# Kernel tuning notes

Hardware: AMD Instinct MI355X
Metric: run time of the kernel (lower is better)

Reference implementation:

```python
import jax, jax.numpy as jnp
import numpy as np
import math

V, D, H, L, MLP = 32000, 1024, 16, 4, 4
B, T = 2, 1024
HD = D // H
ALIBI_BIAS_MAX = 8.0
EPS = 1e-5


def _ln(x, g, b):
    m = jnp.mean(x, -1, keepdims=True)
    v = jnp.mean((x - m) ** 2, -1, keepdims=True)
    return (x - m) * jax.lax.rsqrt(v + EPS) * g + b


def setup_inputs() -> dict:
    key = jax.random.key(0)
    ks = jax.random.split(key, 12)
    s = 0.02
    inp = {
        "input_ids": jax.random.randint(ks[0], (B, T), 0, V),
        "wte": jax.random.normal(ks[1], (V, D), jnp.float32) * s,
        "ln1_g": jnp.ones((L, D), jnp.float32),
        "ln1_b": jnp.zeros((L, D), jnp.float32),
        "attn_w": jax.random.normal(ks[2], (L, 3 * D, D), jnp.float32) * s,
        "attn_b": jnp.zeros((L, 3 * D), jnp.float32),
        "proj_w": jax.random.normal(ks[3], (L, D, D), jnp.float32) * s,
        "proj_b": jnp.zeros((L, D), jnp.float32),
        "ln2_g": jnp.ones((L, D), jnp.float32),
        "ln2_b": jnp.zeros((L, D), jnp.float32),
        "fc_w": jax.random.normal(ks[4], (L, MLP * D, D), jnp.float32) * s,
        "fc_b": jnp.zeros((L, MLP * D), jnp.float32),
        "fc2_w": jax.random.normal(ks[5], (L, D, MLP * D), jnp.float32) * s,
        "fc2_b": jnp.zeros((L, D), jnp.float32),
        "lnf_g": jnp.ones((D,), jnp.float32),
        "lnf_b": jnp.zeros((D,), jnp.float32),
        "lm_head_w": jax.random.normal(ks[6], (V, D), jnp.float32) * s,
    }
    return inp


def reference(input_ids, wte, ln1_g, ln1_b, attn_w, attn_b, proj_w, proj_b,
              ln2_g, ln2_b, fc_w, fc_b, fc2_w, fc2_b, lnf_g, lnf_b, lm_head_w):
    b, t = input_ids.shape
    x = wte[input_ids]  # [B,T,D]

    # causal + ALiBi bias, [H,T,T]
    pos = jnp.arange(t)
    rel = -jnp.abs(pos[None, :] - pos[:, None]).astype(jnp.float32)  # -|i-j|
    m = jnp.arange(1, H + 1, dtype=jnp.float32) * (ALIBI_BIAS_MAX / H)
    alibi = rel[None, :, :] * (2.0 ** (-m))[:, None, None]
    causal = jnp.where(pos[None, :] > pos[:, None], -jnp.inf, 0.0)
    bias = alibi + causal[None]
    scale = 1.0 / math.sqrt(HD)

    def block(x, p):
        l1g, l1b, aw, ab, pw, pb, l2g, l2b, fw, fb, f2w, f2b = p
        h = _ln(x, l1g, l1b)
        qkv = h @ aw.T + ab  # [B,T,3D]
        q, k, v = jnp.split(qkv, 3, axis=-1)
        q = q.reshape(b, t, H, HD).transpose(0, 2, 1, 3)
        k = k.reshape(b, t, H, HD).transpose(0, 2, 1, 3)
        v = v.reshape(b, t, H, HD).transpose(0, 2, 1, 3)
        att = jnp.einsum('bhid,bhjd->bhij', q, k) * scale + bias[None]
        att = jax.nn.softmax(att, axis=-1)
        y = jnp.einsum('bhij,bhjd->bhid', att, v)
        y = y.transpose(0, 2, 1, 3).reshape(b, t, D)
        x = x + (y @ pw.T + pb)
        h2 = _ln(x, l2g, l2b)
        x = x + (jax.nn.gelu(h2 @ fw.T + fb, approximate=False) @ f2w.T + f2b)
        return x, None

    x, _ = jax.lax.scan(
        block, x,
        (ln1_g, ln1_b, attn_w, attn_b, proj_w, proj_b,
         ln2_g, ln2_b, fc_w, fc_b, fc2_w, fc2_b))
    x = _ln(x, lnf_g, lnf_b)
    logits = x @ lm_head_w.T  # [B,T,V]
    return logits
```

## Files before the change

### kernel.cpp

```cpp
#include <hip/hip_runtime.h>
#include <hip/hip_bf16.h>
#include <math.h>

typedef __hip_bfloat16 bf16;
typedef __attribute__((ext_vector_type(4))) float f32x4;
typedef __attribute__((ext_vector_type(8))) short short8;

constexpr int Bc = 2, Tc = 1024, Dc = 1024, Hc = 16, Lc = 4, MLPc = 4096, Vc = 32000, HDc = 64;

__device__ __forceinline__ unsigned short f2bu(float f) {
    __hip_bfloat16 h = __float2bfloat16(f);
    unsigned short u;
    __builtin_memcpy(&u, &h, 2);
    return u;
}

__device__ __forceinline__ void gl2lds16(const bf16* g, bf16* l) {
    __builtin_amdgcn_global_load_lds(
        (const __attribute__((address_space(1))) void*)g,
        (__attribute__((address_space(3))) void*)l, 16, 0, 0);
}

enum { EPI_BIAS_BF16 = 0, EPI_GELU = 1, EPI_RESADD = 2, EPI_F32 = 3, EPI_QKV = 4 };

template <int EPI>
__device__ __forceinline__ void epi_store(float v, int row, int col, void* Cv,
                                          int ldc, const float* bias) {
    if constexpr (EPI == EPI_BIAS_BF16) {
        v += bias[col];
        ((bf16*)Cv)[(size_t)row * ldc + col] = __float2bfloat16(v);
    } else if constexpr (EPI == EPI_GELU) {
        v += bias[col];
        v = 0.5f * v * (1.0f + erff(v * 0.70710678118f));
        ((bf16*)Cv)[(size_t)row * ldc + col] = __float2bfloat16(v);
    } else if constexpr (EPI == EPI_RESADD) {
        float* C = (float*)Cv;
        size_t idx = (size_t)row * ldc + col;
        C[idx] += v + bias[col];
    } else if constexpr (EPI == EPI_F32) {
        ((float*)Cv)[(size_t)row * ldc + col] = v;
    } else if constexpr (EPI == EPI_QKV) {
        v += bias[col];
        bf16 bv = __float2bfloat16(v);
        int b = row >> 10, t = row & 1023;
        int seg = col >> 10;
        int cc = col & 1023;
        int h = cc >> 6, hd = cc & 63;
        bf16* base = (bf16*)Cv;
        if (seg == 0)
            base[((size_t)(b * Hc + h) * Tc + t) * HDc + hd] = bv;
        else if (seg == 1)
            base[2097152 + ((size_t)(b * Hc + h) * Tc + t) * HDc + hd] = bv;
        else
            base[4194304 + ((size_t)(b * Hc + h) * HDc + hd) * Tc + t] = bv;
    }
}

template <int MH>
__device__ __forceinline__ void load_af8(short8 (&af)[4][2], const char* Abase,
                                         int wm, int lr, int lq) {
#pragma unroll
    for (int fi = 0; fi < 4; fi++) {
        int r = MH * 128 + wm * 64 + fi * 16 + lr;
#pragma unroll
        for (int kk = 0; kk < 2; kk++) {
            int cb = (kk * 64 + lq * 16) ^ ((r & 7) << 4);
            af[fi][kk] = *reinterpret_cast<const short8*>(Abase + (size_t)r * 128 + cb);
        }
    }
}
template <int NH>
__device__ __forceinline__ void load_bf4(short8 (&bfv)[2][2], const char* Bbase,
                                         int wn, int lr, int lq) {
#pragma unroll
    for (int fj = 0; fj < 2; fj++) {
        int r = NH * 128 + wn * 32 + fj * 16 + lr;
#pragma unroll
        for (int kk = 0; kk < 2; kk++) {
            int cb = (kk * 64 + lq * 16) ^ ((r & 7) << 4);
            bfv[fj][kk] = *reinterpret_cast<const short8*>(Bbase + (size_t)r * 128 + cb);
        }
    }
}
template <int MH, int NH>
__device__ __forceinline__ void mma16(f32x4 (&acc)[2][2][4][2],
                                      const short8 (&af)[4][2], const short8 (&bfv)[2][2]) {
#pragma unroll
    for (int kk = 0; kk < 2; kk++)
#pragma unroll
        for (int fi = 0; fi < 4; fi++)
#pragma unroll
            for (int fj = 0; fj < 2; fj++)
                acc[MH][NH][fi][fj] = __builtin_amdgcn_mfma_f32_16x16x32_bf16(
                    af[fi][kk], bfv[fj][kk], acc[MH][NH][fi][fj], 0, 0, 0);
}

template <int EPI>
__global__ __launch_bounds__(512) void gemm_8p(
    const bf16* __restrict__ A, int lda,
    const bf16* __restrict__ Bm, int ldb,
    void* __restrict__ Cv, int ldc,
    const float* __restrict__ bias, int K)
{
    constexpr int BM = 256, BN = 256, BK = 64;
    __shared__ alignas(16) bf16 As[2][BM][BK];
    __shared__ alignas(16) bf16 Bs[2][BN][BK];

    const int tid = threadIdx.x;
    const int lane = tid & 63;
    const int w = tid >> 6;
    const int wm = w >> 2;
    const int wn = w & 3;

    int nwg = gridDim.x * gridDim.y;
    int orig = blockIdx.y * gridDim.x + blockIdx.x;
    int q = nwg >> 3, rr = nwg & 7, xcd = orig & 7, lid = orig >> 3;
    int wg = (xcd < rr ? xcd * (q + 1) : rr * (q + 1) + (xcd - rr) * q) + lid;
    int im = wg % gridDim.x;
    int in = wg / gridDim.x;

    const bf16* Ab = A + (size_t)im * BM * lda;
    const bf16* Bb = Bm + (size_t)in * BN * ldb;

    const int sr = lane >> 3;
    const int scs = ((lane & 7) ^ sr) * 8;
    const int lr = lane & 15, lq = lane >> 4;

    f32x4 acc[2][2][4][2];
#pragma unroll
    for (int a = 0; a < 2; a++)
#pragma unroll
        for (int b = 0; b < 2; b++)
#pragma unroll
            for (int c = 0; c < 4; c++)
#pragma unroll
                for (int d = 0; d < 2; d++) acc[a][b][c][d] = (f32x4){0.f, 0.f, 0.f, 0.f};

    const int NT = K / BK;

    auto stage_half = [&](int buf, int sg, int k0) {
        const bool isB = (sg == 1 || sg == 2);
        const bf16* gp = isB ? Bb : Ab;
        const int ld = isB ? ldb : lda;
        bf16* ls = isB ? &Bs[buf][0][0] : &As[buf][0][0];
        const int half = (sg == 2 || sg == 3) ? 1 : 0;
#pragma unroll
        for (int i = 0; i < 2; i++) {
            int r0 = half * 128 + i * 64 + w * 8;
            gl2lds16(gp + (size_t)(r0 + sr) * ld + k0 + scs, ls + r0 * BK);
        }
    };

#pragma unroll
    for (int sg = 0; sg < 4; sg++) stage_half(0, sg, 0);
    asm volatile("s_waitcnt vmcnt(0)" ::: "memory");
    __builtin_amdgcn_s_barrier();
    asm volatile("" ::: "memory");

    short8 af[4][2], bfv[2][2];

    for (int t = 0; t < NT; t++) {
        const int cur = t & 1;
        const char* Abase = (const char*)&As[cur][0][0];
        const char* Bbase = (const char*)&Bs[cur][0][0];
        const bool pf = (t + 1 < NT);
        const int kn = (t + 1) * BK;

        load_af8<0>(af, Abase, wm, lr, lq);
        load_bf4<0>(bfv, Bbase, wn, lr, lq);
        if (pf) stage_half(cur ^ 1, 0, kn);
        __builtin_amdgcn_s_barrier();
        __builtin_amdgcn_s_setprio(1);
        mma16<0, 0>(acc, af, bfv);
        __builtin_amdgcn_s_setprio(0);
        asm volatile("s_waitcnt vmcnt(4)" ::: "memory");
        __builtin_amdgcn_s_barrier();

        load_bf4<1>(bfv, Bbase, wn, lr, lq);
        if (pf) stage_half(cur ^ 1, 1, kn);
        __builtin_amdgcn_s_barrier();
        __builtin_amdgcn_s_setprio(1);
        mma16<0, 1>(acc, af, bfv);
        __builtin_amdgcn_s_setprio(0);
        asm volatile("s_waitcnt vmcnt(4)" ::: "memory");
        __builtin_amdgcn_s_barrier();

        load_af8<1>(af, Abase, wm, lr, lq);
        if (pf) stage_half(cur ^ 1, 2, kn);
        __builtin_amdgcn_s_barrier();
        __builtin_amdgcn_s_setprio(1);
        mma16<1, 1>(acc, af, bfv);
        __builtin_amdgcn_s_setprio(0);
        asm volatile("" ::: "memory");
        __builtin_amdgcn_s_barrier();

        load_bf4<0>(bfv, Bbase, wn, lr, lq);
        if (pf) stage_half(cur ^ 1, 3, kn);
        __builtin_amdgcn_s_barrier();
        __builtin_amdgcn_s_setprio(1);
        mma16<1, 0>(acc, af, bfv);
        __builtin_amdgcn_s_setprio(0);
        asm volatile("s_waitcnt vmcnt(4)" ::: "memory");
        __builtin_amdgcn_s_barrier();
    }

#pragma unroll
    for (int mh = 0; mh < 2; mh++)
#pragma unroll
        for (int nh = 0; nh < 2; nh++)
#pragma unroll
            for (int fi = 0; fi < 4; fi++)
#pragma unroll
                for (int fj = 0; fj < 2; fj++)
#pragma unroll
                    for (int r = 0; r < 4; r++) {
                        int row = im * 256 + mh * 128 + wm * 64 + fi * 16 + lq * 4 + r;
                        int col = in * 256 + nh * 128 + wn * 32 + fj * 16 + lr;
                        epi_store<EPI>(acc[mh][nh][fi][fj][r], row, col, Cv, ldc, bias);
                    }
}

template <int BM, int BN, int BK, int EPI, bool SWZG>
__global__ __launch_bounds__(256) void gemm_fast(
    const bf16* __restrict__ A, int lda,
    const bf16* __restrict__ Bm, int ldb,
    void* __restrict__ Cv, int ldc,
    const float* __restrict__ bias, int K)
{
    static_assert(BK == 64, "staging geometry assumes BK=64");
    __shared__ alignas(16) bf16 As[2][BM][BK];
    __shared__ alignas(16) bf16 Bs[2][BN][BK];

    const int tid = threadIdx.x;
    const int lane = tid & 63;
    const int w = tid >> 6;
    const int wm = w >> 1, wn = w & 1;
    constexpr int WM = BM / 2, WN = BN / 2;
    constexpr int FM = WM / 16, FN = WN / 16;
    constexpr int RPI = 512 / BK;
    constexpr int AI = BM / (4 * RPI);
    constexpr int BI = BN / (4 * RPI);

    int im, in;
    if constexpr (SWZG) {
        int nwg = gridDim.x * gridDim.y;
        int orig = blockIdx.y * gridDim.x + blockIdx.x;
        int q = nwg >> 3, rr = nwg & 7, xcd = orig & 7, lid = orig >> 3;
        int wg = (xcd < rr ? xcd * (q + 1) : rr * (q + 1) + (xcd - rr) * q) + lid;
        im = wg % gridDim.x;
        in = wg / gridDim.x;
    } else {
        im = blockIdx.y;
        in = blockIdx.x;
    }

    const bf16* Ab = A + (size_t)im * BM * lda;
    const bf16* Bb = Bm + (size_t)in * BN * ldb;

    const int sr = lane >> 3;
    const int scs = (((lane & 7) ^ sr) * 8);
    const int lr = lane & 15, lq = lane >> 4;

    f32x4 acc[FM][FN];
#pragma unroll
    for (int i = 0; i < FM; i++)
#pragma unroll
        for (int j = 0; j < FN; j++) acc[i][j] = (f32x4){0.f, 0.f, 0.f, 0.f};

    auto stage = [&](int buf, int k0) {
#pragma unroll
        for (int i = 0; i < AI; i++) {
            int row = (w * AI + i) * RPI;
            gl2lds16(Ab + (size_t)(row + sr) * lda + k0 + scs, &As[buf][row][0]);
        }
#pragma unroll
        for (int i = 0; i < BI; i++) {
            int row = (w * BI + i) * RPI;
            gl2lds16(Bb + (size_t)(row + sr) * ldb + k0 + scs, &Bs[buf][row][0]);
        }
    };

    const int NT = K / BK;
    stage(0, 0);
    __syncthreads();

    for (int t = 0; t < NT; t++) {
        const int cur = t & 1;
        if (t + 1 < NT) stage(cur ^ 1, (t + 1) * BK);

        const char* Abase = (const char*)&As[cur][0][0];
        const char* Bbase = (const char*)&Bs[cur][0][0];
#pragma unroll
        for (int kk = 0; kk < BK / 32; kk++) {
            short8 af[FM], bfr[FN];
#pragma unroll
            for (int i = 0; i < FM; i++) {
                int r = wm * WM + i * 16 + lr;
                int cb = (kk * 64 + lq * 16) ^ ((r & 7) << 4);
                af[i] = *reinterpret_cast<const short8*>(Abase + (size_t)r * (BK * 2) + cb);
            }
#pragma unroll
            for (int j = 0; j < FN; j++) {
                int r = wn * WN + j * 16 + lr;
                int cb = (kk * 64 + lq * 16) ^ ((r & 7) << 4);
                bfr[j] = *reinterpret_cast<const short8*>(Bbase + (size_t)r * (BK * 2) + cb);
            }
#pragma unroll
            for (int i = 0; i < FM; i++)
#pragma unroll
                for (int j = 0; j < FN; j++)
                    acc[i][j] = __builtin_amdgcn_mfma_f32_16x16x32_bf16(af[i], bfr[j], acc[i][j], 0, 0, 0);
        }
        __syncthreads();
    }

#pragma unroll
    for (int i = 0; i < FM; i++)
#pragma unroll
        for (int j = 0; j < FN; j++)
#pragma unroll
            for (int r = 0; r < 4; r++) {
                int row = im * BM + wm * WM + i * 16 + lq * 4 + r;
                int col = in * BN + wn * WN + j * 16 + lr;
                epi_store<EPI>(acc[i][j][r], row, col, Cv, ldc, bias);
            }
}

template <int BM, int BN, int BK, int EPI>
__global__ __launch_bounds__(256) void gemm_bt_f32(
    const bf16* __restrict__ A, int lda,
    const float* __restrict__ Bm, int ldb,
    void* __restrict__ Cv, int ldc,
    const float* __restrict__ bias, int K)
{
    constexpr int BKP = BK + 8;
    __shared__ bf16 As[BM][BKP];
    __shared__ bf16 Bs[BN][BKP];
    const int tid = threadIdx.x;
    const int lane = tid & 63;
    const int w = tid >> 6;
    const int wm = w >> 1, wn = w & 1;
    constexpr int WM = BM / 2, WN = BN / 2;
    constexpr int FM = WM / 16, FN = WN / 16;
    const int bx = blockIdx.x, by = blockIdx.y;
    const bf16* Ab = A + (size_t)by * BM * lda;
    const float* Bb = Bm + (size_t)bx * BN * ldb;
    f32x4 acc[FM][FN];
#pragma unroll
    for (int i = 0; i < FM; i++)
#pragma unroll
        for (int j = 0; j < FN; j++) acc[i][j] = (f32x4){0.f, 0.f, 0.f, 0.f};
    const int lr = lane & 15, lq = lane >> 4;
    for (int k0 = 0; k0 < K; k0 += BK) {
        constexpr int AC = (BM * BK) / (256 * 8);
#pragma unroll
        for (int i = 0; i < AC; i++) {
            int c = tid + i * 256;
            int row = c / (BK / 8);
            int kc = (c % (BK / 8)) * 8;
            *reinterpret_cast<int4*>(&As[row][kc]) =
                *reinterpret_cast<const int4*>(Ab + (size_t)row * lda + k0 + kc);
        }
        constexpr int BC = (BN * BK) / (256 * 4);
#pragma unroll
        for (int i = 0; i < BC; i++) {
            int c = tid + i * 256;
            int row = c / (BK / 4);
            int kc = (c % (BK / 4)) * 4;
            float4 v = *reinterpret_cast<const float4*>(Bb + (size_t)row * ldb + k0 + kc);
            unsigned long long p = (unsigned long long)f2bu(v.x) |
                                   ((unsigned long long)f2bu(v.y) << 16) |
                                   ((unsigned long long)f2bu(v.z) << 32) |
                                   ((unsigned long long)f2bu(v.w) << 48);
            *reinterpret_cast<unsigned long long*>(&Bs[row][kc]) = p;
        }
        __syncthreads();
#pragma unroll
        for (int kk = 0; kk < BK / 32; kk++) {
            short8 af[FM], bfr[FN];
#pragma unroll
            for (int i = 0; i < FM; i++)
                af[i] = *reinterpret_cast<const short8*>(&As[wm * WM + i * 16 + lr][kk * 32 + lq * 8]);
#pragma unroll
            for (int j = 0; j < FN; j++)
                bfr[j] = *reinterpret_cast<const short8*>(&Bs[wn * WN + j * 16 + lr][kk * 32 + lq * 8]);
#pragma unroll
            for (int i = 0; i < FM; i++)
#pragma unroll
                for (int j = 0; j < FN; j++)
                    acc[i][j] = __builtin_amdgcn_mfma_f32_16x16x32_bf16(af[i], bfr[j], acc[i][j], 0, 0, 0);
        }
        __syncthreads();
    }
#pragma unroll
    for (int i = 0; i < FM; i++)
#pragma unroll
        for (int j = 0; j < FN; j++)
#pragma unroll
            for (int r = 0; r < 4; r++) {
                int row = by * BM + wm * WM + i * 16 + lq * 4 + r;
                int col = bx * BN + wn * WN + j * 16 + lr;
                epi_store<EPI>(acc[i][j][r], row, col, Cv, ldc, bias);
            }
}

__global__ __launch_bounds__(256) void flash_attn(
    const bf16* __restrict__ q, const bf16* __restrict__ kbuf,
    const bf16* __restrict__ vt, bf16* __restrict__ y)
{
    __shared__ alignas(16) bf16 Ks[128 * 64];
    __shared__ alignas(16) bf16 Vs[64 * 128];
    __shared__ alignas(16) bf16 Ps[4 * 16 * 136];

    const int tid = threadIdx.x;
    const int lane = tid & 63;
    const int w = tid >> 6;
    const int lr = lane & 15, lq = lane >> 4;
    const int qi = (int)gridDim.x - 1 - (int)blockIdx.x;
    const int z = blockIdx.y;
    const int b = z >> 4, h = z & 15;
    const float slope = exp2f(-0.5f * (float)(h + 1));

    const bf16* qz = q + (size_t)z * (Tc * HDc);
    const bf16* kz = kbuf + (size_t)z * (Tc * HDc);
    const bf16* vz = vt + (size_t)z * (HDc * Tc);

    const int rowbase = qi * 64 + w * 16;

    short8 qf[2];
#pragma unroll
    for (int kk = 0; kk < 2; kk++)
        qf[kk] = *reinterpret_cast<const short8*>(
            qz + (size_t)(rowbase + lr) * HDc + kk * 32 + lq * 8);

    float m_old[4], l_sum[4];
#pragma unroll
    for (int r = 0; r < 4; r++) { m_old[r] = -3.0e38f; l_sum[r] = 0.f; }
    f32x4 o[4];
#pragma unroll
    for (int dj = 0; dj < 4; dj++) o[dj] = (f32x4){0.f, 0.f, 0.f, 0.f};

    bf16* Pw = Ps + w * 16 * 136;

    const int nkv = (qi * 64 + 63) / 128 + 1;
    for (int kv = 0; kv < nkv; kv++) {
#pragma unroll
        for (int i = 0; i < 4; i++) {
            int rbase = w * 32 + i * 8;
            int row = rbase + (lane >> 3);
            int slot = lane & 7;
            gl2lds16(kz + (size_t)(kv * 128 + row) * HDc + ((slot ^ (row & 7)) * 8),
                     &Ks[rbase * 64]);
        }
#pragma unroll
        for (int i = 0; i < 4; i++) {
            int rbase = w * 16 + i * 4;
            int row = rbase + lq;
            gl2lds16(vz + (size_t)row * Tc + kv * 128 + ((lr ^ (row & 7)) * 8),
                     &Vs[rbase * 128]);
        }
        __syncthreads();

        f32x4 s[8];
#pragma unroll
        for (int j = 0; j < 8; j++) s[j] = (f32x4){0.f, 0.f, 0.f, 0.f};
#pragma unroll
        for (int kk = 0; kk < 2; kk++) {
#pragma unroll
            for (int j = 0; j < 8; j++) {
                int row = j * 16 + lr;
                int cb = ((kk * 4 + lq) ^ (row & 7)) << 4;
                short8 bfr = *reinterpret_cast<const short8*>(
                    (const char*)Ks + row * 128 + cb);
                s[j] = __builtin_amdgcn_mfma_f32_16x16x32_bf16(qf[kk], bfr, s[j], 0, 0, 0);
            }
        }

        float mt[4];
#pragma unroll
        for (int r = 0; r < 4; r++) mt[r] = -3.0e38f;
#pragma unroll
        for (int j = 0; j < 8; j++) {
            int col = kv * 128 + j * 16 + lr;
#pragma unroll
            for (int r = 0; r < 4; r++) {
                int rowg = rowbase + lq * 4 + r;
                float v = s[j][r] * 0.125f - (float)(rowg - col) * slope;
                v = (col > rowg) ? -3.0e38f : v;
                s[j][r] = v;
                mt[r] = fmaxf(mt[r], v);
            }
        }
#pragma unroll
        for (int r = 0; r < 4; r++)
#pragma unroll
            for (int off = 1; off < 16; off <<= 1)
                mt[r] = fmaxf(mt[r], __shfl_xor(mt[r], off));

        float f[4], rs[4];
#pragma unroll
        for (int r = 0; r < 4; r++) {
            float mn = fmaxf(m_old[r], mt[r]);
            f[r] = __expf(m_old[r] - mn);
            m_old[r] = mn;
            rs[r] = 0.f;
        }
#pragma unroll
        for (int j = 0; j < 8; j++)
#pragma unroll
            for (int r = 0; r < 4; r++) {
                float p = __expf(s[j][r] - m_old[r]);
                s[j][r] = p;
                rs[r] += p;
            }
#pragma unroll
        for (int r = 0; r < 4; r++) {
#pragma unroll
            for (int off = 1; off < 16; off <<= 1)
                rs[r] += __shfl_xor(rs[r], off);
            l_sum[r] = l_sum[r] * f[r] + rs[r];
        }

#pragma unroll
        for (int j = 0; j < 8; j++)
#pragma unroll
            for (int r = 0; r < 4; r++)
                Pw[(lq * 4 + r) * 136 + j * 16 + lr] = __float2bfloat16(s[j][r]);

#pragma unroll
        for (int dj = 0; dj < 4; dj++)
#pragma unroll
            for (int r = 0; r < 4; r++) o[dj][r] *= f[r];

        __syncthreads();

#pragma unroll
        for (int kk = 0; kk < 4; kk++) {
            short8 pa = *reinterpret_cast<const short8*>(
                (const char*)Pw + lr * 272 + kk * 64 + lq * 16);
#pragma unroll
            for (int dj = 0; dj < 4; dj++) {
                int row = dj * 16 + lr;
                int cb = ((kk * 4 + lq) ^ (row & 7)) << 4;
                short8 vb = *reinterpret_cast<const short8*>(
                    (const char*)Vs + row * 256 + cb);
                o[dj] = __builtin_amdgcn_mfma_f32_16x16x32_bf16(pa, vb, o[dj], 0, 0, 0);
            }
        }
        __syncthreads();
    }

#pragma unroll
    for (int dj = 0; dj < 4; dj++)
#pragma unroll
        for (int r = 0; r < 4; r++) {
            int rowg = rowbase + lq * 4 + r;
            float outv = o[dj][r] / l_sum[r];
            y[((size_t)b * Tc + rowg) * Dc + h * HDc + dj * 16 + lr] =
                __float2bfloat16(outv);
        }
}

__global__ __launch_bounds__(256) void f2b8(const float* __restrict__ in,
                                            bf16* __restrict__ out, long n) {
    long i = ((long)blockIdx.x * 256 + threadIdx.x) * 8;
    if (i >= n) return;
    float4 a = *reinterpret_cast<const float4*>(in + i);
    float4 b = *reinterpret_cast<const float4*>(in + i + 4);
    unsigned long long p0 = (unsigned long long)f2bu(a.x) |
                            ((unsigned long long)f2bu(a.y) << 16) |
                            ((unsigned long long)f2bu(a.z) << 32) |
                            ((unsigned long long)f2bu(a.w) << 48);
    unsigned long long p1 = (unsigned long long)f2bu(b.x) |
                            ((unsigned long long)f2bu(b.y) << 16) |
                            ((unsigned long long)f2bu(b.z) << 32) |
                            ((unsigned long long)f2bu(b.w) << 48);
    *reinterpret_cast<unsigned long long*>(out + i) = p0;
    *reinterpret_cast<unsigned long long*>(out + i + 4) = p1;
}

__global__ __launch_bounds__(256) void embed_kernel(const int* __restrict__ ids,
                                                    const float* __restrict__ wte,
                                                    float* __restrict__ x) {
    int row = blockIdx.x;
    int t = threadIdx.x;
    int id = ids[row];
    reinterpret_cast<float4*>(x + (size_t)row * Dc)[t] =
        reinterpret_cast<const float4*>(wte + (size_t)id * Dc)[t];
}

__global__ __launch_bounds__(256) void ln_kernel(const float* __restrict__ x,
                                                 const float* __restrict__ g,
                                                 const float* __restrict__ b,
                                                 bf16* __restrict__ out) {
    int row = blockIdx.x;
    int t = threadIdx.x;
    const float4 v = reinterpret_cast<const float4*>(x + (size_t)row * Dc)[t];
    float s = v.x + v.y + v.z + v.w;
    float s2 = v.x * v.x + v.y * v.y + v.z * v.z + v.w * v.w;
#pragma unroll
    for (int o = 32; o > 0; o >>= 1) {
        s += __shfl_down(s, o);
        s2 += __shfl_down(s2, o);
    }
    __shared__ float sm[8];
    int wid = t >> 6, ln = t & 63;
    if (ln == 0) { sm[wid] = s; sm[4 + wid] = s2; }
    __syncthreads();
    if (t == 0) {
        float ts = sm[0] + sm[1] + sm[2] + sm[3];
        float ts2 = sm[4] + sm[5] + sm[6] + sm[7];
        sm[0] = ts; sm[4] = ts2;
    }
    __syncthreads();
    float mean = sm[0] * (1.0f / Dc);
    float var = sm[4] * (1.0f / Dc) - mean * mean;
    float rstd = rsqrtf(var + 1e-5f);
    int c0 = t * 4;
    float vv[4] = {v.x, v.y, v.z, v.w};
    unsigned long long p = 0;
#pragma unroll
    for (int j = 0; j < 4; j++) {
        float val = (vv[j] - mean) * rstd * g[c0 + j] + b[c0 + j];
        p |= (unsigned long long)f2bu(val) << (16 * j);
    }
    *reinterpret_cast<unsigned long long*>(out + (size_t)row * Dc + c0) = p;
}

extern "C" void kernel_launch(void* const* d_in, const int* in_sizes, int n_in,
                              void* d_out, int out_size, void* d_ws, size_t ws_size,
                              hipStream_t stream) {
    const int* ids = (const int*)d_in[0];
    const float* wte = (const float*)d_in[1];
    const float* ln1g = (const float*)d_in[2];
    const float* ln1b = (const float*)d_in[3];
    const float* attw = (const float*)d_in[4];
    const float* attb = (const float*)d_in[5];
    const float* projw = (const float*)d_in[6];
    const float* projb = (const float*)d_in[7];
    const float* ln2g = (const float*)d_in[8];
    const float* ln2b = (const float*)d_in[9];
    const float* fcw = (const float*)d_in[10];
    const float* fcb = (const float*)d_in[11];
    const float* fc2w = (const float*)d_in[12];
    const float* fc2b = (const float*)d_in[13];
    const float* lnfg = (const float*)d_in[14];
    const float* lnfb = (const float*)d_in[15];
    const float* lmw = (const float*)d_in[16];

    const int M = Bc * Tc;
    char* ws = (char*)d_ws;
    size_t off = 0;
    auto carve = [&](size_t bytes) { char* p = ws + off; off += (bytes + 255) & ~(size_t)255; return p; };

    float* x = (float*)carve((size_t)M * Dc * 4);
    bf16* h = (bf16*)carve((size_t)M * Dc * 2);
    bf16* q = (bf16*)carve((size_t)Bc * Hc * Tc * HDc * 2);
    bf16* kb = (bf16*)carve((size_t)Bc * Hc * Tc * HDc * 2);
    bf16* vt = (bf16*)carve((size_t)Bc * Hc * Tc * HDc * 2);
    bf16* y = (bf16*)carve((size_t)M * Dc * 2);
    bf16* mlp = (bf16*)carve((size_t)M * MLPc * 2);
    (void)kb; (void)vt;

    const long nLM = (long)Vc * Dc;
    bool has_wlm = ws_size >= off + (size_t)nLM * 2;
    bf16* wlm = nullptr;
    if (has_wlm) wlm = (bf16*)carve((size_t)nLM * 2);

    const long nAW = (long)Lc * 3 * Dc * Dc;
    const long nPW = (long)Lc * Dc * Dc;
    const long nFW = (long)Lc * MLPc * Dc;
    const long nF2W = (long)Lc * Dc * MLPc;
    bf16* awAll = (bf16*)d_out;
    bf16* pwAll = awAll + nAW;
    bf16* fwAll = pwAll + nPW;
    bf16* f2wAll = fwAll + nFW;

    embed_kernel<<<M, 256, 0, stream>>>(ids, wte, x);

    f2b8<<<(int)(nAW / 8 / 256), 256, 0, stream>>>(attw, awAll, nAW);
    f2b8<<<(int)(nPW / 8 / 256), 256, 0, stream>>>(projw, pwAll, nPW);
    f2b8<<<(int)(nFW / 8 / 256), 256, 0, stream>>>(fcw, fwAll, nFW);
    f2b8<<<(int)(nF2W / 8 / 256), 256, 0, stream>>>(fc2w, f2wAll, nF2W);
    if (has_wlm)
        f2b8<<<(int)(nLM / 8 / 256), 256, 0, stream>>>(lmw, wlm, nLM);

    for (int l = 0; l < Lc; l++) {
        bf16* aw_b = awAll + (size_t)l * 3 * Dc * Dc;
        bf16* pw_b = pwAll + (size_t)l * Dc * Dc;
        bf16* fw_b = fwAll + (size_t)l * MLPc * Dc;
        bf16* f2w_b = f2wAll + (size_t)l * Dc * MLPc;

        ln_kernel<<<M, 256, 0, stream>>>(x, ln1g + l * Dc, ln1b + l * Dc, h);

        gemm_fast<128, 128, 64, EPI_QKV, true>
            <<<dim3(M / 128, 3 * Dc / 128, 1), 256, 0, stream>>>(
                h, Dc, aw_b, Dc, q, 0, attb + l * 3 * Dc, Dc);

        flash_attn<<<dim3(Tc / 64, Bc * Hc), 256, 0, stream>>>(q, kb, vt, y);

        gemm_fast<128, 128, 64, EPI_RESADD, true>
            <<<dim3(M / 128, Dc / 128, 1), 256, 0, stream>>>(
                y, Dc, pw_b, Dc, x, Dc, projb + l * Dc, Dc);

        ln_kernel<<<M, 256, 0, stream>>>(x, ln2g + l * Dc, ln2b + l * Dc, h);

        gemm_fast<128, 128, 64, EPI_GELU, true>
            <<<dim3(M / 128, MLPc / 128, 1), 256, 0, stream>>>(
                h, Dc, fw_b, Dc, mlp, MLPc, fcb + l * MLPc, Dc);

        gemm_fast<128, 128, 64, EPI_RESADD, true>
            <<<dim3(M / 128, Dc / 128, 1), 256, 0, stream>>>(
                mlp, MLPc, f2w_b, MLPc, x, Dc, fc2b + l * Dc, MLPc);
    }

    ln_kernel<<<M, 256, 0, stream>>>(x, lnfg, lnfb, h);

    if (has_wlm)
        gemm_8p<EPI_F32>
            <<<dim3(M / 256, Vc / 256, 1), 512, 0, stream>>>(
                h, Dc, wlm, Dc, (float*)d_out, Vc, nullptr, Dc);
    else
        gemm_bt_f32<128, 128, 64, EPI_F32>
            <<<dim3(Vc / 128, M / 128, 1), 256, 0, stream>>>(
                h, Dc, lmw, Dc, (float*)d_out, Vc, nullptr, Dc);
}
```

Measured before the change: 1.282 ms.

## Store residual stream in bf16, add V transpose kernel, reuse B fragments

The residual stream x moves from fp32 to bf16 storage, so embed, layernorm and the residual-add epilogues read and write half the bytes. The QKV epilogue now writes V in the same row-major layout as Q and K, and a separate v2vt kernel transposes it for flash attention instead of doing strided scattered stores. The GEMM main loop keeps two B fragment register sets, which removes one LDS reload per k-step at the cost of more registers. Rounding the residual to bf16 after every layer adds accumulated precision error against the fp32 reference.

```diff
diff --git a/kernel.cpp b/kernel.cpp
--- a/kernel.cpp
+++ b/kernel.cpp
@@ -13,6 +13,11 @@
     unsigned short u;
     __builtin_memcpy(&u, &h, 2);
     return u;
+}
+__device__ __forceinline__ float bu2f(unsigned short u) {
+    __hip_bfloat16 h;
+    __builtin_memcpy(&h, &u, 2);
+    return __bfloat162float(h);
 }
 
 __device__ __forceinline__ void gl2lds16(const bf16* g, bf16* l) {
@@ -34,9 +39,10 @@
         v = 0.5f * v * (1.0f + erff(v * 0.70710678118f));
         ((bf16*)Cv)[(size_t)row * ldc + col] = __float2bfloat16(v);
     } else if constexpr (EPI == EPI_RESADD) {
-        float* C = (float*)Cv;
+        bf16* C = (bf16*)Cv;
         size_t idx = (size_t)row * ldc + col;
-        C[idx] += v + bias[col];
+        float xo = __bfloat162float(C[idx]);
+        C[idx] = __float2bfloat16(xo + v + bias[col]);
     } else if constexpr (EPI == EPI_F32) {
         ((float*)Cv)[(size_t)row * ldc + col] = v;
     } else if constexpr (EPI == EPI_QKV) {
@@ -47,12 +53,7 @@
         int cc = col & 1023;
         int h = cc >> 6, hd = cc & 63;
         bf16* base = (bf16*)Cv;
-        if (seg == 0)
-            base[((size_t)(b * Hc + h) * Tc + t) * HDc + hd] = bv;
-        else if (seg == 1)
-            base[2097152 + ((size_t)(b * Hc + h) * Tc + t) * HDc + hd] = bv;
-        else
-            base[4194304 + ((size_t)(b * Hc + h) * HDc + hd) * Tc + t] = bv;
+        base[(size_t)seg * 2097152 + ((size_t)(b * Hc + h) * Tc + t) * HDc + hd] = bv;
     }
 }
 
@@ -157,7 +158,7 @@
     __builtin_amdgcn_s_barrier();
     asm volatile("" ::: "memory");
 
-    short8 af[4][2], bfv[2][2];
+    short8 af[4][2], bfv0[2][2], bfv1[2][2];
 
     for (int t = 0; t < NT; t++) {
         const int cur = t & 1;
@@ -167,20 +168,20 @@
         const int kn = (t + 1) * BK;
 
         load_af8<0>(af, Abase, wm, lr, lq);
-        load_bf4<0>(bfv, Bbase, wn, lr, lq);
+        load_bf4<0>(bfv0, Bbase, wn, lr, lq);
         if (pf) stage_half(cur ^ 1, 0, kn);
         __builtin_amdgcn_s_barrier();
         __builtin_amdgcn_s_setprio(1);
-        mma16<0, 0>(acc, af, bfv);
+        mma16<0, 0>(acc, af, bfv0);
         __builtin_amdgcn_s_setprio(0);
         asm volatile("s_waitcnt vmcnt(4)" ::: "memory");
         __builtin_amdgcn_s_barrier();
 
-        load_bf4<1>(bfv, Bbase, wn, lr, lq);
+        load_bf4<1>(bfv1, Bbase, wn, lr, lq);
         if (pf) stage_half(cur ^ 1, 1, kn);
         __builtin_amdgcn_s_barrier();
         __builtin_amdgcn_s_setprio(1);
-        mma16<0, 1>(acc, af, bfv);
+        mma16<0, 1>(acc, af, bfv1);
         __builtin_amdgcn_s_setprio(0);
         asm volatile("s_waitcnt vmcnt(4)" ::: "memory");
         __builtin_amdgcn_s_barrier();
@@ -189,16 +190,15 @@
         if (pf) stage_half(cur ^ 1, 2, kn);
         __builtin_amdgcn_s_barrier();
         __builtin_amdgcn_s_setprio(1);
-        mma16<1, 1>(acc, af, bfv);
+        mma16<1, 1>(acc, af, bfv1);
         __builtin_amdgcn_s_setprio(0);
         asm volatile("" ::: "memory");
         __builtin_amdgcn_s_barrier();
 
-        load_bf4<0>(bfv, Bbase, wn, lr, lq);
         if (pf) stage_half(cur ^ 1, 3, kn);
         __builtin_amdgcn_s_barrier();
         __builtin_amdgcn_s_setprio(1);
-        mma16<1, 0>(acc, af, bfv);
+        mma16<1, 0>(acc, af, bfv0);
         __builtin_amdgcn_s_setprio(0);
         asm volatile("s_waitcnt vmcnt(4)" ::: "memory");
         __builtin_amdgcn_s_barrier();
@@ -581,23 +581,31 @@
 
 __global__ __launch_bounds__(256) void embed_kernel(const int* __restrict__ ids,
                                                     const float* __restrict__ wte,
-                                                    float* __restrict__ x) {
+                                                    bf16* __restrict__ x) {
     int row = blockIdx.x;
     int t = threadIdx.x;
     int id = ids[row];
-    reinterpret_cast<float4*>(x + (size_t)row * Dc)[t] =
-        reinterpret_cast<const float4*>(wte + (size_t)id * Dc)[t];
-}
-
-__global__ __launch_bounds__(256) void ln_kernel(const float* __restrict__ x,
+    float4 v = reinterpret_cast<const float4*>(wte + (size_t)id * Dc)[t];
+    unsigned long long p = (unsigned long long)f2bu(v.x) |
+                           ((unsigned long long)f2bu(v.y) << 16) |
+                           ((unsigned long long)f2bu(v.z) << 32) |
+                           ((unsigned long long)f2bu(v.w) << 48);
+    *reinterpret_cast<unsigned long long*>(x + (size_t)row * Dc + t * 4) = p;
+}
+
+__global__ __launch_bounds__(256) void ln_kernel(const bf16* __restrict__ x,
                                                  const float* __restrict__ g,
                                                  const float* __restrict__ b,
                                                  bf16* __restrict__ out) {
     int row = blockIdx.x;
     int t = threadIdx.x;
-    const float4 v = reinterpret_cast<const float4*>(x + (size_t)row * Dc)[t];
-    float s = v.x + v.y + v.z + v.w;
-    float s2 = v.x * v.x + v.y * v.y + v.z * v.z + v.w * v.w;
+    unsigned long long uv = *reinterpret_cast<const unsigned long long*>(
+        x + (size_t)row * Dc + t * 4);
+    float vv[4];
+#pragma unroll
+    for (int j = 0; j < 4; j++) vv[j] = bu2f((unsigned short)(uv >> (16 * j)));
+    float s = vv[0] + vv[1] + vv[2] + vv[3];
+    float s2 = vv[0] * vv[0] + vv[1] * vv[1] + vv[2] * vv[2] + vv[3] * vv[3];
 #pragma unroll
     for (int o = 32; o > 0; o >>= 1) {
         s += __shfl_down(s, o);
@@ -617,7 +625,6 @@
     float var = sm[4] * (1.0f / Dc) - mean * mean;
     float rstd = rsqrtf(var + 1e-5f);
     int c0 = t * 4;
-    float vv[4] = {v.x, v.y, v.z, v.w};
     unsigned long long p = 0;
 #pragma unroll
     for (int j = 0; j < 4; j++) {
@@ -625,6 +632,33 @@
         p |= (unsigned long long)f2bu(val) << (16 * j);
     }
     *reinterpret_cast<unsigned long long*>(out + (size_t)row * Dc + c0) = p;
+}
+
+__global__ __launch_bounds__(256) void v2vt(const bf16* __restrict__ v,
+                                            bf16* __restrict__ vt) {
+    int idx = blockIdx.x * 256 + threadIdx.x;
+    int tc = idx & 127;
+    int t0 = tc * 8;
+    int rest = idx >> 7;
+    int hd = rest & 63;
+    int z = rest >> 6;
+    const bf16* src = v + ((size_t)z * Tc) * HDc + hd;
+    unsigned long long p0 = 0, p1 = 0;
+#pragma unroll
+    for (int i = 0; i < 4; i++) {
+        unsigned short u;
+        __builtin_memcpy(&u, src + (size_t)(t0 + i) * HDc, 2);
+        p0 |= (unsigned long long)u << (16 * i);
+    }
+#pragma unroll
+    for (int i = 0; i < 4; i++) {
+        unsigned short u;
+        __builtin_memcpy(&u, src + (size_t)(t0 + 4 + i) * HDc, 2);
+        p1 |= (unsigned long long)u << (16 * i);
+    }
+    bf16* dst = vt + ((size_t)z * HDc + hd) * Tc + t0;
+    *reinterpret_cast<unsigned long long*>(dst) = p0;
+    *reinterpret_cast<unsigned long long*>(dst + 4) = p1;
 }
 
 extern "C" void kernel_launch(void* const* d_in, const int* in_sizes, int n_in,
@@ -653,14 +687,15 @@
     size_t off = 0;
     auto carve = [&](size_t bytes) { char* p = ws + off; off += (bytes + 255) & ~(size_t)255; return p; };
 
-    float* x = (float*)carve((size_t)M * Dc * 4);
+    bf16* x = (bf16*)carve((size_t)M * Dc * 2);
     bf16* h = (bf16*)carve((size_t)M * Dc * 2);
-    bf16* q = (bf16*)carve((size_t)Bc * Hc * Tc * HDc * 2);
-    bf16* kb = (bf16*)carve((size_t)Bc * Hc * Tc * HDc * 2);
-    bf16* vt = (bf16*)carve((size_t)Bc * Hc * Tc * HDc * 2);
+    bf16* qkvb = (bf16*)carve((size_t)3 * 2097152 * 2);
+    bf16* vt = (bf16*)carve((size_t)Bc * Hc * HDc * Tc * 2);
     bf16* y = (bf16*)carve((size_t)M * Dc * 2);
     bf16* mlp = (bf16*)carve((size_t)M * MLPc * 2);
-    (void)kb; (void)vt;
+    bf16* q = qkvb;
+    bf16* kb = qkvb + 2097152;
+    bf16* vtmp = qkvb + 4194304;
 
     const long nLM = (long)Vc * Dc;
     bool has_wlm = ws_size >= off + (size_t)nLM * 2;
@@ -695,7 +730,9 @@
 
         gemm_fast<128, 128, 64, EPI_QKV, true>
             <<<dim3(M / 128, 3 * Dc / 128, 1), 256, 0, stream>>>(
-                h, Dc, aw_b, Dc, q, 0, attb + l * 3 * Dc, Dc);
+                h, Dc, aw_b, Dc, qkvb, 0, attb + l * 3 * Dc, Dc);
+
+        v2vt<<<(Bc * Hc * HDc * (Tc / 8)) / 256, 256, 0, stream>>>(vtmp, vt);
 
         flash_attn<<<dim3(Tc / 64, Bc * Hc), 256, 0, stream>>>(q, kb, vt, y);
 
```

After: 1.250 ms. -2.5%, faster.
